# Optimization experiments

Measured on AMD Instinct MI355X. Metric: run time of the kernel, lower is better.

The kernel has to match this reference:

```python
import jax, jax.numpy as jnp
import numpy as np

BS, SL, ENC_DIM, EDGE_DIM = 8, 256, 1024, 256
MINUS_INF = -1.0e8


def setup_inputs() -> dict:
    key = jax.random.key(0)
    ks = jax.random.split(key, 5)
    encoded_text = jax.random.normal(ks[0], (BS, SL, ENC_DIM), dtype=jnp.float32)
    mask = jnp.ones((BS, SL), dtype=jnp.int64)
    # Linear params (torch stores weight as (out, in)); scale like default init
    Wh = jax.random.normal(ks[1], (EDGE_DIM, ENC_DIM), dtype=jnp.float32) / np.sqrt(ENC_DIM)
    bh = jax.random.normal(ks[2], (EDGE_DIM,), dtype=jnp.float32) / np.sqrt(ENC_DIM)
    Wc = jax.random.normal(ks[3], (EDGE_DIM, ENC_DIM), dtype=jnp.float32) / np.sqrt(ENC_DIM)
    w_out = jax.random.normal(ks[4], (EDGE_DIM,), dtype=jnp.float32) / np.sqrt(EDGE_DIM)
    return {"encoded_text": encoded_text, "mask": mask, "Wh": Wh, "bh": bh, "Wc": Wc, "w_out": w_out}


def reference(encoded_text, mask, Wh, bh, Wc, w_out):
    # head/child projections: (bs, sl, edge_dim)
    head = jnp.einsum('bse,de->bsd', encoded_text, Wh) + bh
    child = jnp.einsum('bse,de->bsd', encoded_text, Wc)
    # Pairwise: torch code gives combined[b,i,j] = tanh(head[b,j] + child[b,i])
    combined = jnp.tanh(head[:, None, :, :] + child[:, :, None, :])  # (bs, sl, sl, edge_dim)
    edge_scores = jnp.einsum('bijd,d->bij', combined, w_out)  # (bs, sl, sl)
    float_mask = mask.astype(jnp.float32)
    minus_mask = (1.0 - float_mask) * MINUS_INF  # (bs, sl)
    edge_scores = edge_scores + minus_mask[:, :, None] + minus_mask[:, None, :]
    return edge_scores
```

## Files before the change

kernel.cpp:

```cpp
#include <hip/hip_runtime.h>
#include <hip/hip_bf16.h>
#include <stdint.h>


typedef __bf16 bf16_t;
typedef __attribute__((ext_vector_type(8))) __bf16 bf16x8;
typedef __attribute__((ext_vector_type(4))) float f32x4;
typedef __attribute__((ext_vector_type(4))) uint32_t u32x4;

#define SL 256
#define ENC 1024
#define NTOT 512
#define KSCALE 2.8853900817779268f
#define LSTR 260

__device__ __forceinline__ uint32_t bfpack(float a, float b) {
  uint32_t ua = __float_as_uint(a); ua = ua + 0x7FFFu + ((ua >> 16) & 1u);
  uint32_t ub = __float_as_uint(b); ub = ub + 0x7FFFu + ((ub >> 16) & 1u);
  return (ua >> 16) | (ub & 0xFFFF0000u);
}

__global__ __launch_bounds__(512)
void projc_kernel(const float* __restrict__ enc, const float* __restrict__ Wh,
                  const float* __restrict__ Wc, const float* __restrict__ bh,
                  float* __restrict__ hc) {
  __shared__ bf16_t As[2][4096];
  __shared__ bf16_t Bs[2][4096];
  const int t = threadIdx.x;
  const int wv = t >> 6, lane = t & 63;
  const int m0 = blockIdx.x * 64;
  const int n0 = blockIdx.y * 64;
  const int srow = t >> 3;
  const int sch = (t & 7) * 8;
  const int mq = (wv & 3) * 16;
  const int nq = (wv >> 2) * 32;
  const int fr = lane & 15, kq = lane >> 4;

  f32x4 acc0 = {0.f, 0.f, 0.f, 0.f};
  f32x4 acc1 = acc0;

  const float* gA = enc + (size_t)(m0 + srow) * ENC + sch;
  const float* gW = ((n0 < 256) ? Wh + (size_t)(n0 + srow) * ENC
                                : Wc + (size_t)(n0 - 256 + srow) * ENC) + sch;

  f32x4 a0 = *(const f32x4*)(gA);
  f32x4 a1 = *(const f32x4*)(gA + 4);
  f32x4 w0 = *(const f32x4*)(gW);
  f32x4 w1 = *(const f32x4*)(gW + 4);

#pragma unroll 2
  for (int i = 0; i < 16; ++i) {
    const int buf = i & 1;
    f32x4 na0, na1, nw0, nw1;
    if (i + 1 < 16) {
      const int k1 = (i + 1) * 64;
      na0 = *(const f32x4*)(gA + k1);
      na1 = *(const f32x4*)(gA + k1 + 4);
      nw0 = *(const f32x4*)(gW + k1);
      nw1 = *(const f32x4*)(gW + k1 + 4);
    } else {
      na0 = a0; na1 = a1; nw0 = w0; nw1 = w1;
    }
    u32x4 Au = {bfpack(a0[0], a0[1]), bfpack(a0[2], a0[3]),
                bfpack(a1[0], a1[1]), bfpack(a1[2], a1[3])};
    u32x4 Wu = {bfpack(w0[0], w0[1]), bfpack(w0[2], w0[3]),
                bfpack(w1[0], w1[1]), bfpack(w1[2], w1[3])};
    *(u32x4*)&As[buf][t * 8] = Au;
    *(u32x4*)&Bs[buf][t * 8] = Wu;
    __syncthreads();
    bf16x8 fa0 = *(const bf16x8*)&As[buf][(mq + fr) * 64 + kq * 8];
    bf16x8 fa1 = *(const bf16x8*)&As[buf][(mq + fr) * 64 + 32 + kq * 8];
    bf16x8 fb00 = *(const bf16x8*)&Bs[buf][(nq + fr) * 64 + kq * 8];
    bf16x8 fb01 = *(const bf16x8*)&Bs[buf][(nq + fr) * 64 + 32 + kq * 8];
    bf16x8 fb10 = *(const bf16x8*)&Bs[buf][(nq + 16 + fr) * 64 + kq * 8];
    bf16x8 fb11 = *(const bf16x8*)&Bs[buf][(nq + 16 + fr) * 64 + 32 + kq * 8];
    acc0 = __builtin_amdgcn_mfma_f32_16x16x32_bf16(fa0, fb00, acc0, 0, 0, 0);
    acc1 = __builtin_amdgcn_mfma_f32_16x16x32_bf16(fa0, fb10, acc1, 0, 0, 0);
    acc0 = __builtin_amdgcn_mfma_f32_16x16x32_bf16(fa1, fb01, acc0, 0, 0, 0);
    acc1 = __builtin_amdgcn_mfma_f32_16x16x32_bf16(fa1, fb11, acc1, 0, 0, 0);
    a0 = na0; a1 = na1; w0 = nw0; w1 = nw1;
  }
  const int colA = n0 + nq + fr;
  const int colB = colA + 16;
  const float biasA = (colA < 256) ? bh[colA] : 0.0f;
  const float biasB = (colB < 256) ? bh[colB] : 0.0f;
#pragma unroll
  for (int r = 0; r < 4; ++r) {
    int row = m0 + mq + kq * 4 + r;
    hc[(size_t)row * NTOT + colA] = __builtin_amdgcn_exp2f(KSCALE * (acc0[r] + biasA));
    hc[(size_t)row * NTOT + colB] = __builtin_amdgcn_exp2f(KSCALE * (acc1[r] + biasB));
  }
}

__global__ __launch_bounds__(256)
void edge_kernel(const float* __restrict__ hc, const float* __restrict__ wout,
                 const int* __restrict__ mask, float* __restrict__ out) {
  __shared__ float ldH[32 * LSTR];
  __shared__ float ldC[32 * LSTR];
  __shared__ float wS[256];
  __shared__ float red[4];
  const int t = threadIdx.x;
  const int lane = t & 63, wv = t >> 6;
  const int b = blockIdx.z;
  const int i0 = blockIdx.y * 32;
  const int j0 = blockIdx.x * 32;
  const int sbase = b * SL;

  float w = wout[t];
  wS[t] = -2.0f * w;
  float wsum = w;
#pragma unroll
  for (int off = 32; off; off >>= 1) wsum += __shfl_xor(wsum, off);
  if (lane == 0) red[wv] = wsum;

  for (int u = t; u < 32 * 64; u += 256) {
    int row = u >> 6;
    int c4 = (u & 63) << 2;
    f32x4 hv = *(const f32x4*)&hc[(size_t)(sbase + j0 + row) * NTOT + c4];
    f32x4 cv = *(const f32x4*)&hc[(size_t)(sbase + i0 + row) * NTOT + 256 + c4];
    *(f32x4*)&ldH[row * LSTR + c4] = hv;
    *(f32x4*)&ldC[row * LSTR + c4] = cv;
  }
  __syncthreads();
  const float S = (red[0] + red[1]) + (red[2] + red[3]);

  const int tx = t & 15, ty = t >> 4;
  const float* hp0 = &ldH[tx * LSTR];
  const float* hp1 = &ldH[(tx + 16) * LSTR];
  const float* cp0 = &ldC[ty * LSTR];
  const float* cp1 = &ldC[(ty + 16) * LSTR];
  float a00 = 0.f, a01 = 0.f, a10 = 0.f, a11 = 0.f;

#pragma unroll 8
  for (int d = 0; d < 256; d += 4) {
    f32x4 h0 = *(const f32x4*)&hp0[d];
    f32x4 h1 = *(const f32x4*)&hp1[d];
    f32x4 c0 = *(const f32x4*)&cp0[d];
    f32x4 c1 = *(const f32x4*)&cp1[d];
    f32x4 w4 = *(const f32x4*)&wS[d];
#pragma unroll
    for (int e = 0; e < 4; ++e) {
      float he0 = h0[e], he1 = h1[e], ce0 = c0[e], ce1 = c1[e], we = w4[e];
      float r00 = __builtin_amdgcn_rcpf(ce0 * he0 + 1.0f);
      float r01 = __builtin_amdgcn_rcpf(ce0 * he1 + 1.0f);
      float r10 = __builtin_amdgcn_rcpf(ce1 * he0 + 1.0f);
      float r11 = __builtin_amdgcn_rcpf(ce1 * he1 + 1.0f);
      a00 = fmaf(we, r00, a00);
      a01 = fmaf(we, r01, a01);
      a10 = fmaf(we, r10, a10);
      a11 = fmaf(we, r11, a11);
    }
  }

  const int gi0 = sbase + i0 + ty, gi1 = gi0 + 16;
  const int gj0 = j0 + tx, gj1 = gj0 + 16;
  const float mi0 = (1.0f - (float)mask[gi0]) * -1.0e8f;
  const float mi1 = (1.0f - (float)mask[gi1]) * -1.0e8f;
  const float mj0 = (1.0f - (float)mask[sbase + gj0]) * -1.0e8f;
  const float mj1 = (1.0f - (float)mask[sbase + gj1]) * -1.0e8f;
  out[(size_t)gi0 * SL + gj0] = S + a00 + mi0 + mj0;
  out[(size_t)gi0 * SL + gj1] = S + a01 + mi0 + mj1;
  out[(size_t)gi1 * SL + gj0] = S + a10 + mi1 + mj0;
  out[(size_t)gi1 * SL + gj1] = S + a11 + mi1 + mj1;
}

extern "C" void kernel_launch(void* const* d_in, const int* in_sizes, int n_in,
                              void* d_out, int out_size, void* d_ws, size_t ws_size,
                              hipStream_t stream) {
  (void)in_sizes; (void)n_in; (void)out_size; (void)ws_size;
  const float* enc = (const float*)d_in[0];
  const int* mask = (const int*)d_in[1];
  const float* Wh = (const float*)d_in[2];
  const float* bh = (const float*)d_in[3];
  const float* Wc = (const float*)d_in[4];
  const float* wout = (const float*)d_in[5];
  float* out = (float*)d_out;

  float* hc = (float*)d_ws;

  projc_kernel<<<dim3(32, 8), 512, 0, stream>>>(enc, Wh, Wc, bh, hc);
  edge_kernel<<<dim3(8, 8, 8), 256, 0, stream>>>(hc, wout, mask, out);
}
```

Before: 98.41 us.

## Double-buffer edge kernel H/C tiles in 64-wide d chunks

The edge kernel no longer loads full 256-wide H and C rows into LDS up front. It streams them in four 64-column chunks through two LDS buffers, prefetching the next chunk while the rcp/FMA loop runs on the current one. This shrinks the kernel's LDS footprint and overlaps global loads with compute, at the cost of extra barriers per block. The new row stride of 66 floats is not a multiple of 4, so the 16-byte vector LDS accesses land on addresses that are not 16-byte aligned, which could split or slow those accesses.

Result: slower. 139.9 us (+42.2%).

```diff
diff --git a/kernel.cpp b/kernel.cpp
--- a/kernel.cpp
+++ b/kernel.cpp
@@ -12,7 +12,8 @@
 #define ENC 1024
 #define NTOT 512
 #define KSCALE 2.8853900817779268f
-#define LSTR 260
+#define DCH 64
+#define ESTR 66
 
 __device__ __forceinline__ uint32_t bfpack(float a, float b) {
   uint32_t ua = __float_as_uint(a); ua = ua + 0x7FFFu + ((ua >> 16) & 1u);
@@ -95,8 +96,8 @@
 __global__ __launch_bounds__(256)
 void edge_kernel(const float* __restrict__ hc, const float* __restrict__ wout,
                  const int* __restrict__ mask, float* __restrict__ out) {
-  __shared__ float ldH[32 * LSTR];
-  __shared__ float ldC[32 * LSTR];
+  __shared__ float ldH[2][32 * ESTR];
+  __shared__ float ldC[2][32 * ESTR];
   __shared__ float wS[256];
   __shared__ float red[4];
   const int t = threadIdx.x;
@@ -113,43 +114,63 @@
   for (int off = 32; off; off >>= 1) wsum += __shfl_xor(wsum, off);
   if (lane == 0) red[wv] = wsum;
 
-  for (int u = t; u < 32 * 64; u += 256) {
-    int row = u >> 6;
-    int c4 = (u & 63) << 2;
-    f32x4 hv = *(const f32x4*)&hc[(size_t)(sbase + j0 + row) * NTOT + c4];
-    f32x4 cv = *(const f32x4*)&hc[(size_t)(sbase + i0 + row) * NTOT + 256 + c4];
-    *(f32x4*)&ldH[row * LSTR + c4] = hv;
-    *(f32x4*)&ldC[row * LSTR + c4] = cv;
+  const float* __restrict__ hbase = &hc[(size_t)(sbase + j0) * NTOT];
+  const float* __restrict__ cbase = &hc[(size_t)(sbase + i0) * NTOT + 256];
+
+#pragma unroll
+  for (int u = t; u < 512; u += 256) {
+    int row = u >> 4;
+    int c4 = (u & 15) << 2;
+    *(f32x4*)&ldH[0][row * ESTR + c4] = *(const f32x4*)&hbase[(size_t)row * NTOT + c4];
+    *(f32x4*)&ldC[0][row * ESTR + c4] = *(const f32x4*)&cbase[(size_t)row * NTOT + c4];
   }
   __syncthreads();
   const float S = (red[0] + red[1]) + (red[2] + red[3]);
 
   const int tx = t & 15, ty = t >> 4;
-  const float* hp0 = &ldH[tx * LSTR];
-  const float* hp1 = &ldH[(tx + 16) * LSTR];
-  const float* cp0 = &ldC[ty * LSTR];
-  const float* cp1 = &ldC[(ty + 16) * LSTR];
   float a00 = 0.f, a01 = 0.f, a10 = 0.f, a11 = 0.f;
 
+  for (int db = 0; db < 4; ++db) {
+    const int cur = db & 1;
+    if (db < 3) {
+      const int nxt = cur ^ 1;
+      const int doff = (db + 1) * DCH;
+#pragma unroll
+      for (int u = t; u < 512; u += 256) {
+        int row = u >> 4;
+        int c4 = (u & 15) << 2;
+        *(f32x4*)&ldH[nxt][row * ESTR + c4] =
+            *(const f32x4*)&hbase[(size_t)row * NTOT + doff + c4];
+        *(f32x4*)&ldC[nxt][row * ESTR + c4] =
+            *(const f32x4*)&cbase[(size_t)row * NTOT + doff + c4];
+      }
+    }
+    const float* hp0 = &ldH[cur][tx * ESTR];
+    const float* hp1 = &ldH[cur][(tx + 16) * ESTR];
+    const float* cp0 = &ldC[cur][ty * ESTR];
+    const float* cp1 = &ldC[cur][(ty + 16) * ESTR];
+    const float* wp = &wS[db * DCH];
 #pragma unroll 8
-  for (int d = 0; d < 256; d += 4) {
-    f32x4 h0 = *(const f32x4*)&hp0[d];
-    f32x4 h1 = *(const f32x4*)&hp1[d];
-    f32x4 c0 = *(const f32x4*)&cp0[d];
-    f32x4 c1 = *(const f32x4*)&cp1[d];
-    f32x4 w4 = *(const f32x4*)&wS[d];
-#pragma unroll
-    for (int e = 0; e < 4; ++e) {
-      float he0 = h0[e], he1 = h1[e], ce0 = c0[e], ce1 = c1[e], we = w4[e];
-      float r00 = __builtin_amdgcn_rcpf(ce0 * he0 + 1.0f);
-      float r01 = __builtin_amdgcn_rcpf(ce0 * he1 + 1.0f);
-      float r10 = __builtin_amdgcn_rcpf(ce1 * he0 + 1.0f);
-      float r11 = __builtin_amdgcn_rcpf(ce1 * he1 + 1.0f);
-      a00 = fmaf(we, r00, a00);
-      a01 = fmaf(we, r01, a01);
-      a10 = fmaf(we, r10, a10);
-      a11 = fmaf(we, r11, a11);
+    for (int d = 0; d < DCH; d += 4) {
+      f32x4 h0 = *(const f32x4*)&hp0[d];
+      f32x4 h1 = *(const f32x4*)&hp1[d];
+      f32x4 c0 = *(const f32x4*)&cp0[d];
+      f32x4 c1 = *(const f32x4*)&cp1[d];
+      f32x4 w4 = *(const f32x4*)&wp[d];
+#pragma unroll
+      for (int e = 0; e < 4; ++e) {
+        float he0 = h0[e], he1 = h1[e], ce0 = c0[e], ce1 = c1[e], we = w4[e];
+        float r00 = __builtin_amdgcn_rcpf(ce0 * he0 + 1.0f);
+        float r01 = __builtin_amdgcn_rcpf(ce0 * he1 + 1.0f);
+        float r10 = __builtin_amdgcn_rcpf(ce1 * he0 + 1.0f);
+        float r11 = __builtin_amdgcn_rcpf(ce1 * he1 + 1.0f);
+        a00 = fmaf(we, r00, a00);
+        a01 = fmaf(we, r01, a01);
+        a10 = fmaf(we, r10, a10);
+        a11 = fmaf(we, r11, a11);
+      }
     }
+    if (db < 3) __syncthreads();
   }
 
   const int gi0 = sbase + i0 + ty, gi1 = gi0 + 16;
```
